# Kernel tuning notes

Hardware: AMD Instinct MI355X
Metric: run time of the kernel (lower is better)

The kernel has to match this reference:

```python
import jax, jax.numpy as jnp
import numpy as np

D_MODEL = 1024
NHEADS = 16
D_K = D_MODEL // NHEADS


def setup_inputs() -> dict:
    key = jax.random.key(0)
    ks = jax.random.split(key, 12)
    B, S = 2, 2048
    scale = 1.0 / np.sqrt(D_MODEL)
    inp = {
        "query": jax.random.normal(ks[0], (B, S, D_MODEL), dtype=jnp.float32),
        "key": jax.random.normal(ks[1], (B, S, D_MODEL), dtype=jnp.float32),
        "value": jax.random.normal(ks[2], (B, S, D_MODEL), dtype=jnp.float32),
        "mask": jax.random.randint(ks[3], (B, 1, S, S), 0, 2, dtype=jnp.int32),
        "Wq": jax.random.normal(ks[4], (D_MODEL, D_MODEL), dtype=jnp.float32) * scale,
        "bq": jnp.zeros((D_MODEL,), dtype=jnp.float32),
        "Wk": jax.random.normal(ks[5], (D_MODEL, D_MODEL), dtype=jnp.float32) * scale,
        "bk": jnp.zeros((D_MODEL,), dtype=jnp.float32),
        "Wv": jax.random.normal(ks[6], (D_MODEL, D_MODEL), dtype=jnp.float32) * scale,
        "bv": jnp.zeros((D_MODEL,), dtype=jnp.float32),
        "Wo": jax.random.normal(ks[7], (D_MODEL, D_MODEL), dtype=jnp.float32) * scale,
        "bo": jnp.zeros((D_MODEL,), dtype=jnp.float32),
    }
    return inp


def _split_heads(x):
    # [B, S, (H*D)] -> [B, H, S, D]
    B, S, _ = x.shape
    return x.reshape(B, S, NHEADS, D_K).transpose(0, 2, 1, 3)


def reference(query, key, value, mask, Wq, bq, Wk, bk, Wv, bv, Wo, bo):
    B, Sq, _ = query.shape
    q = _split_heads(query @ Wq + bq)            # [B, H, Sq, Dk]
    k = _split_heads(key @ Wk + bk)              # [B, H, Sk, Dk]
    v = _split_heads(value @ Wv + bv)            # [B, H, Sk, Dk]
    # scores: [B, H, Sq, Sk], scaled by sqrt(d_k)
    scores = jnp.einsum("bhqd,bhkd->bhqk", q, k) / np.sqrt(D_K).astype(np.float32)
    scores = jnp.where(mask == 0, jnp.float32(-1e12), scores)
    weights = jax.nn.softmax(scores, axis=-1)
    out = jnp.einsum("bhqk,bhkd->bhqd", weights, v)  # [B, H, Sq, Dk]
    out = out.transpose(0, 2, 1, 3).reshape(B, Sq, D_MODEL)
    return out @ Wo + bo  # dropout is identity in eval / p=0
```

## Files before the change

kernel.cpp:

```cpp
#include <hip/hip_runtime.h>
#include <math.h>

#define D_MODEL 1024
#define NHEADS  16
#define DK      64
#define BATCH   2
#define SEQ     2048
#define M_TOTAL (BATCH * SEQ)
#define NT      (SEQ / 64)
#define QSCALE 0.18033688011112042f

typedef __attribute__((ext_vector_type(8))) short bf16x8;
typedef __attribute__((ext_vector_type(4))) float f32x4;

__device__ __forceinline__ unsigned short f2bf(float f) {
    union { float f; unsigned int i; } v; v.f = f;
    return (unsigned short)((v.i + 0x7FFFu + ((v.i >> 16) & 1u)) >> 16);
}

__device__ __forceinline__ void async_copy16(const void* g, void* l) {
    __builtin_amdgcn_global_load_lds(
        (const __attribute__((address_space(1))) unsigned int*)g,
        (__attribute__((address_space(3))) unsigned int*)l, 16, 0, 0);
}

struct PrepArgs {
    const float* xs[3]; unsigned short* xd[3];
    const float* wsrc[4]; unsigned short* wdst[4];
    const int* mask; unsigned long long* wm;
};

__global__ __launch_bounds__(256)
void prep_all(const PrepArgs a)
{
    __shared__ unsigned short tbuf[32][33];
    const int id  = blockIdx.x;
    const int tid = threadIdx.x;

    if (id < 12288) {
        const int z = id >> 12;
        const int x = id & 4095;
        const float* __restrict__ s = a.xs[z];
        unsigned short* __restrict__ d = a.xd[z];
        const size_t i = ((size_t)x * 256 + tid) * 4;
        const float4 v = *reinterpret_cast<const float4*>(&s[i]);
        ushort4 o;
        o.x = f2bf(v.x); o.y = f2bf(v.y); o.z = f2bf(v.z); o.w = f2bf(v.w);
        *reinterpret_cast<ushort4*>(&d[i]) = o;
    } else if (id < 16384) {
        const int r  = id - 12288;
        const int z  = r >> 10;
        const int rem = r & 1023;
        const int bx = rem & 31;
        const int by = rem >> 5;
        const float* __restrict__ W = a.wsrc[z];
        unsigned short* __restrict__ WT = a.wdst[z];
        const int tx = tid & 31;
        const int ty = tid >> 5;
        const int nb = bx << 5;
        const int kb = by << 5;
#pragma unroll
        for (int i = 0; i < 4; ++i)
            tbuf[ty + (i << 3)][tx] =
                f2bf(W[(size_t)(kb + ty + (i << 3)) * D_MODEL + nb + tx]);
        __syncthreads();
#pragma unroll
        for (int i = 0; i < 4; ++i)
            WT[(size_t)(nb + ty + (i << 3)) * D_MODEL + kb + tx] =
                tbuf[tx][ty + (i << 3)];
    } else {
        const int bxm = id - 16384;
        const int lane = tid & 63;
        const int l15  = lane & 15;
        const int kg   = lane >> 4;
        const int wv   = (bxm << 2) + (tid >> 6);
        const int t    = wv & 31;
        const int qw   = (wv >> 5) & 127;
        const int bb   = wv >> 12;

        const int* mb = a.mask + (size_t)bb * SEQ * SEQ
                      + (size_t)((qw << 4) + l15) * SEQ + (t << 6) + (kg << 2);
        unsigned long long* wout = a.wm + ((((size_t)bb * 128 + qw) * 32 + t) << 4);

        int4 ln[4];
#pragma unroll
        for (int n = 0; n < 4; ++n)
            ln[n] = *reinterpret_cast<const int4*>(mb + (n << 4));
#pragma unroll
        for (int r = 0; r < 4; ++r)
#pragma unroll
            for (int n = 0; n < 4; ++n) {
                const int mvv = (&ln[n].x)[r];
                const unsigned long long bal = __ballot(mvv != 0);
                if (lane == 0) wout[(r << 2) | n] = bal;
            }
    }
}

template <typename OutT> struct GArgs {
    const unsigned short* X[3];
    const unsigned short* W[3];
    const float*          Bi[3];
    OutT*                 O[3];
    float                 scl[3];
};

__device__ __forceinline__ void st_out(float* p, float v) { *p = v; }
__device__ __forceinline__ void st_out(unsigned short* p, float v) { *p = f2bf(v); }

template <typename OutT>
__global__ __launch_bounds__(256)
void gemm_bf16(const GArgs<OutT> args, const int head_split, const int m_z_tiles)
{
    __shared__ __align__(16) unsigned short As[128][32];
    __shared__ __align__(16) unsigned short Bs[128][32];

    const int opz = m_z_tiles ? 0 : blockIdx.z;
    const unsigned short* __restrict__ X  = args.X[opz];
    const unsigned short* __restrict__ WT = args.W[opz];
    const float* __restrict__ bias        = args.Bi[opz];
    OutT* __restrict__ out                = args.O[opz];
    const float scl                       = args.scl[opz];

    const int tid = threadIdx.x;
    const int wid = tid >> 6;
    const int wy  = wid >> 1;
    const int wx  = wid & 1;
    const int l15 = tid & 15;
    const int kg  = (tid >> 4) & 3;

    const int nwgy = (int)gridDim.y;
    const int id = ((int)blockIdx.y << 3) | (int)blockIdx.x;
    const int sw = (id & 7) * nwgy + (id >> 3);
    const int n0 = (sw & 7) << 7;
    const int m0 = ((sw >> 3) + (int)blockIdx.z * m_z_tiles) << 7;

    const int lane = tid & 63;
    const int gr   = lane >> 2;
    const int gc   = (lane & 3) << 3;
    const int c0   = wid << 1;

    f32x4 acc[4][4];
#pragma unroll
    for (int i = 0; i < 4; ++i)
#pragma unroll
        for (int j = 0; j < 4; ++j)
            acc[i][j] = (f32x4){0.f, 0.f, 0.f, 0.f};

#pragma unroll 1
    for (int t = 0; t < D_MODEL / 32; ++t) {
        const int k0 = t << 5;

        __syncthreads();
#pragma unroll
        for (int cc = 0; cc < 2; ++cc) {
            const int c = c0 + cc;
            async_copy16(&X[(size_t)(m0 + (c << 4) + gr) * D_MODEL + k0 + gc],
                         &As[c << 4][0]);
            async_copy16(&WT[(size_t)(n0 + (c << 4) + gr) * D_MODEL + k0 + gc],
                         &Bs[c << 4][0]);
        }
        __syncthreads();

        bf16x8 a[4], b[4];
#pragma unroll
        for (int i = 0; i < 4; ++i)
            a[i] = *reinterpret_cast<const bf16x8*>(
                &As[(wy << 6) + (i << 4) + l15][kg << 3]);
#pragma unroll
        for (int j = 0; j < 4; ++j)
            b[j] = *reinterpret_cast<const bf16x8*>(
                &Bs[(wx << 6) + (j << 4) + l15][kg << 3]);
#pragma unroll
        for (int i = 0; i < 4; ++i)
#pragma unroll
            for (int j = 0; j < 4; ++j)
                acc[i][j] = __builtin_amdgcn_mfma_f32_16x16x32_bf16(
                    a[i], b[j], acc[i][j], 0, 0, 0);
    }

    float bv[4];
#pragma unroll
    for (int j = 0; j < 4; ++j)
        bv[j] = bias[n0 + (wx << 6) + (j << 4) + l15];

#pragma unroll
    for (int i = 0; i < 4; ++i) {
#pragma unroll
        for (int r = 0; r < 4; ++r) {
            const int m = m0 + (wy << 6) + (i << 4) + (kg << 2) + r;
#pragma unroll
            for (int j = 0; j < 4; ++j) {
                const int n = n0 + (wx << 6) + (j << 4) + l15;
                const float val = (acc[i][j][r] + bv[j]) * scl;
                if (head_split) {
                    const int bbx = m >> 11;
                    const int ss  = m & (SEQ - 1);
                    const int hhx = n >> 6;
                    const int dd  = n & (DK - 1);
                    st_out(&out[((size_t)(bbx * NHEADS + hhx) * SEQ + ss) * DK + dd], val);
                } else {
                    st_out(&out[(size_t)m * D_MODEL + n], val);
                }
            }
        }
    }
}

__global__ __launch_bounds__(256)
void flash_mfma(const unsigned short* __restrict__ Qb,
                const unsigned short* __restrict__ Kb,
                const unsigned short* __restrict__ Vb,
                const unsigned long long* __restrict__ wmask,
                unsigned short* __restrict__ ctx)
{
    __shared__ __align__(16) unsigned short Kbf[2][64][72];
    __shared__ __align__(16) unsigned short V3 [2][64][72];

    const int tid  = threadIdx.x;
    const int w    = tid >> 6;
    const int lane = tid & 63;
    const int l15  = lane & 15;
    const int kg   = lane >> 4;

    const int flat = ((int)blockIdx.z * NHEADS + (int)blockIdx.y) * (SEQ / 128)
                   + (int)blockIdx.x;
    const int swz  = ((flat & 7) << 6) | (flat >> 3);
    const int q0 = (swz & 15) << 7;
    const int hh = (swz >> 4) & 15;
    const int bb = swz >> 8;

    const unsigned short* Qh = Qb + (size_t)(bb * NHEADS + hh) * SEQ * DK;
    const unsigned short* Kh = Kb + (size_t)(bb * NHEADS + hh) * SEQ * DK;
    const unsigned short* Vh = Vb + (size_t)(bb * NHEADS + hh) * SEQ * DK;

    bf16x8 aq[2][2];
#pragma unroll
    for (int qi = 0; qi < 2; ++qi) {
        const unsigned short* qrow =
            Qh + (size_t)(q0 + w * 32 + qi * 16 + l15) * DK + (kg << 3);
        aq[qi][0] = *reinterpret_cast<const bf16x8*>(qrow);
        aq[qi][1] = *reinterpret_cast<const bf16x8*>(qrow + 32);
    }

    const int krow = tid >> 2;
    const int kcb  = (tid & 3) << 4;
    const int vkb  = (tid & 15) << 2;
    const int vdb  = (tid >> 4) << 2;
    const int voff = (((vkb >> 2) & 3) << 4) + ((vkb >> 4) << 2);

    const int wbase0 = __builtin_amdgcn_readfirstlane(
        (bb * 128 + (q0 >> 4) + (w << 1)) << 9);
    const int wbase1 = wbase0 + 512;

    f32x4 lsum[2];
    f32x4 O4[2][4];
#pragma unroll
    for (int qi = 0; qi < 2; ++qi) {
        lsum[qi] = (f32x4){0.f, 0.f, 0.f, 0.f};
#pragma unroll
        for (int db = 0; db < 4; ++db) O4[qi][db] = (f32x4){0.f, 0.f, 0.f, 0.f};
    }

    uint4 kv0 = *reinterpret_cast<const uint4*>(Kh + (size_t)krow * DK + kcb);
    uint4 kv1 = *reinterpret_cast<const uint4*>(Kh + (size_t)krow * DK + kcb + 8);
    uint2 vr[4];
#pragma unroll
    for (int i = 0; i < 4; ++i)
        vr[i] = *reinterpret_cast<const uint2*>(Vh + (size_t)(vkb + i) * DK + vdb);

#pragma unroll 1
    for (int t = 0; t < NT; ++t) {
        const int c = t & 1;

        *reinterpret_cast<uint4*>(&Kbf[c][krow][kcb])     = kv0;
        *reinterpret_cast<uint4*>(&Kbf[c][krow][kcb + 8]) = kv1;
        {
            uint2 o;
            o.x = (vr[0].x & 0xFFFFu) | (vr[1].x << 16);
            o.y = (vr[2].x & 0xFFFFu) | (vr[3].x << 16);
            *reinterpret_cast<uint2*>(&V3[c][vdb + 0][voff]) = o;
            o.x = (vr[0].x >> 16) | (vr[1].x & 0xFFFF0000u);
            o.y = (vr[2].x >> 16) | (vr[3].x & 0xFFFF0000u);
            *reinterpret_cast<uint2*>(&V3[c][vdb + 1][voff]) = o;
            o.x = (vr[0].y & 0xFFFFu) | (vr[1].y << 16);
            o.y = (vr[2].y & 0xFFFFu) | (vr[3].y << 16);
            *reinterpret_cast<uint2*>(&V3[c][vdb + 2][voff]) = o;
            o.x = (vr[0].y >> 16) | (vr[1].y & 0xFFFF0000u);
            o.y = (vr[2].y >> 16) | (vr[3].y & 0xFFFF0000u);
            *reinterpret_cast<uint2*>(&V3[c][vdb + 3][voff]) = o;
        }
        __syncthreads();

        if (t + 1 < NT) {
            const int kn = (t + 1) << 6;
            kv0 = *reinterpret_cast<const uint4*>(Kh + (size_t)(kn + krow) * DK + kcb);
            kv1 = *reinterpret_cast<const uint4*>(Kh + (size_t)(kn + krow) * DK + kcb + 8);
#pragma unroll
            for (int i = 0; i < 4; ++i)
                vr[i] = *reinterpret_cast<const uint2*>(
                    Vh + (size_t)(kn + vkb + i) * DK + vdb);
        }

        f32x4 S[2][4];
#pragma unroll
        for (int n = 0; n < 4; ++n) {
            const bf16x8 b0 = *reinterpret_cast<const bf16x8*>(
                &Kbf[c][16 * n + l15][kg << 3]);
            const bf16x8 b1 = *reinterpret_cast<const bf16x8*>(
                &Kbf[c][16 * n + l15][(kg << 3) + 32]);
#pragma unroll
            for (int qi = 0; qi < 2; ++qi) {
                f32x4 acc = (f32x4){0.f, 0.f, 0.f, 0.f};
                acc = __builtin_amdgcn_mfma_f32_16x16x32_bf16(b0, aq[qi][0], acc, 0, 0, 0);
                acc = __builtin_amdgcn_mfma_f32_16x16x32_bf16(b1, aq[qi][1], acc, 0, 0, 0);
                S[qi][n] = acc;
            }
        }

        bf16x8 paf[2][2];
#pragma unroll
        for (int qi = 0; qi < 2; ++qi) {
            const unsigned long long* wmt =
                wmask + (qi ? wbase1 : wbase0) + (t << 4);
            unsigned long long wmv[16];
#pragma unroll
            for (int rn = 0; rn < 16; ++rn) wmv[rn] = wmt[rn];

            unsigned pw01[4], pw23[4];
#pragma unroll
            for (int n = 0; n < 4; ++n) {
                float xv[4];
#pragma unroll
                for (int r = 0; r < 4; ++r) {
                    float e;
                    __asm__("v_exp_f32 %0, %1" : "=v"(e) : "v"(S[qi][n][r]));
                    __asm__("v_cndmask_b32 %0, 0, %1, %2"
                            : "=v"(e) : "v"(e), "s"(wmv[(r << 2) | n]));
                    xv[r] = e;
                }
                lsum[qi][0] += xv[0];
                lsum[qi][1] += xv[1];
                lsum[qi][2] += xv[2];
                lsum[qi][3] += xv[3];
                __asm__("v_cvt_pk_bf16_f32 %0, %1, %2"
                        : "=v"(pw01[n]) : "v"(xv[0]), "v"(xv[1]));
                __asm__("v_cvt_pk_bf16_f32 %0, %1, %2"
                        : "=v"(pw23[n]) : "v"(xv[2]), "v"(xv[3]));
            }
            union { unsigned u[4]; bf16x8 v; } pa0, pa1;
            pa0.u[0] = pw01[0]; pa0.u[1] = pw23[0]; pa0.u[2] = pw01[1]; pa0.u[3] = pw23[1];
            pa1.u[0] = pw01[2]; pa1.u[1] = pw23[2]; pa1.u[2] = pw01[3]; pa1.u[3] = pw23[3];
            paf[qi][0] = pa0.v;
            paf[qi][1] = pa1.v;
        }

#pragma unroll
        for (int db = 0; db < 4; ++db) {
            const unsigned short* vbase = &V3[c][(db << 4) + l15][kg << 4];
            const bf16x8 v0 = *reinterpret_cast<const bf16x8*>(vbase);
            const bf16x8 v1 = *reinterpret_cast<const bf16x8*>(vbase + 8);
#pragma unroll
            for (int qi = 0; qi < 2; ++qi) {
                O4[qi][db] = __builtin_amdgcn_mfma_f32_16x16x32_bf16(
                    paf[qi][0], v0, O4[qi][db], 0, 0, 0);
                O4[qi][db] = __builtin_amdgcn_mfma_f32_16x16x32_bf16(
                    paf[qi][1], v1, O4[qi][db], 0, 0, 0);
            }
        }
    }

#pragma unroll
    for (int qi = 0; qi < 2; ++qi) {
        float ls = (lsum[qi][0] + lsum[qi][1]) + (lsum[qi][2] + lsum[qi][3]);
        ls += __shfl_xor(ls, 16);
        ls += __shfl_xor(ls, 32);
#pragma unroll
        for (int r = 0; r < 4; ++r) {
            const float rs = __shfl(ls, (kg << 2) + r);
            const float inv = 1.f / rs;
            const size_t base =
                (size_t)(bb * SEQ + q0 + w * 32 + qi * 16 + (kg << 2) + r) * D_MODEL
                + hh * DK + l15;
#pragma unroll
            for (int db = 0; db < 4; ++db)
                ctx[base + 16 * db] = f2bf(O4[qi][db][r] * inv);
        }
    }
}

extern "C" void kernel_launch(void* const* d_in, const int* in_sizes, int n_in,
                              void* d_out, int out_size, void* d_ws, size_t ws_size,
                              hipStream_t stream)
{
    const float* query = (const float*)d_in[0];
    const float* key   = (const float*)d_in[1];
    const float* value = (const float*)d_in[2];
    const int*   mask  = (const int*)d_in[3];
    const float* Wq = (const float*)d_in[4];
    const float* bq = (const float*)d_in[5];
    const float* Wk = (const float*)d_in[6];
    const float* bk = (const float*)d_in[7];
    const float* Wv = (const float*)d_in[8];
    const float* bv = (const float*)d_in[9];
    const float* Wo = (const float*)d_in[10];
    const float* bo = (const float*)d_in[11];

    unsigned short* ws = (unsigned short*)d_ws;
    const size_t TE = (size_t)M_TOTAL * D_MODEL;
    const size_t WE = (size_t)D_MODEL * D_MODEL;
    unsigned short* Xq  = ws;
    unsigned short* Xk  = Xq + TE;
    unsigned short* Xv  = Xk + TE;
    unsigned short* WTq = Xv + TE;
    unsigned short* WTk = WTq + WE;
    unsigned short* WTv = WTk + WE;
    unsigned short* WTo = WTv + WE;
    unsigned short* Qb  = WTo + WE;
    unsigned short* Kb  = Qb + TE;
    unsigned short* Vb  = Kb + TE;
    unsigned short* Ctx = Vb + TE;
    unsigned long long* WM = (unsigned long long*)(Ctx + TE);

    PrepArgs pa;
    pa.xs[0] = query; pa.xs[1] = key; pa.xs[2] = value;
    pa.xd[0] = Xq;    pa.xd[1] = Xk;  pa.xd[2] = Xv;
    pa.wsrc[0] = Wq;  pa.wsrc[1] = Wk;  pa.wsrc[2] = Wv;  pa.wsrc[3] = Wo;
    pa.wdst[0] = WTq; pa.wdst[1] = WTk; pa.wdst[2] = WTv; pa.wdst[3] = WTo;
    pa.mask = mask; pa.wm = WM;
    prep_all<<<dim3(18432, 1, 1), 256, 0, stream>>>(pa);

    GArgs<unsigned short> qkv;
    qkv.X[0] = Xq;  qkv.X[1] = Xk;  qkv.X[2] = Xv;
    qkv.W[0] = WTq; qkv.W[1] = WTk; qkv.W[2] = WTv;
    qkv.Bi[0] = bq; qkv.Bi[1] = bk; qkv.Bi[2] = bv;
    qkv.O[0] = Qb;  qkv.O[1] = Kb;  qkv.O[2] = Vb;
    qkv.scl[0] = QSCALE; qkv.scl[1] = 1.f; qkv.scl[2] = 1.f;
    gemm_bf16<unsigned short><<<dim3(8, 32, 3), 256, 0, stream>>>(qkv, 1, 0);

    flash_mfma<<<dim3(SEQ / 128, NHEADS, BATCH), 256, 0, stream>>>(
        Qb, Kb, Vb, WM, Ctx);

    GArgs<float> op;
    op.X[0] = Ctx;  op.X[1] = Ctx;  op.X[2] = Ctx;
    op.W[0] = WTo;  op.W[1] = WTo;  op.W[2] = WTo;
    op.Bi[0] = bo;  op.Bi[1] = bo;  op.Bi[2] = bo;
    op.O[0] = (float*)d_out; op.O[1] = (float*)d_out; op.O[2] = (float*)d_out;
    op.scl[0] = 1.f; op.scl[1] = 1.f; op.scl[2] = 1.f;
    gemm_bf16<float><<<dim3(8, 16, 2), 256, 0, stream>>>(op, 0, 16);
}
```

Measured before the change: 266.0 us.

## Stage 128-key tiles in flash attention and use 64-row tiles for output GEMM

The attention kernel now loads and stages 128 keys per loop iteration, not 64. It halves the number of barriers and loop iterations and prefetches larger K/V blocks, at the cost of more LDS and registers. The GEMM is templated on the number of M sub-tiles, and the output projection uses 64x128 tiles with a single z-slice. This gives twice as many workgroups for better CU occupancy, but each one reuses less data.

New measurement: 258.7 us. 2.8% less time.

```diff
diff --git a/kernel.cpp b/kernel.cpp
--- a/kernel.cpp
+++ b/kernel.cpp
@@ -7,7 +7,7 @@
 #define BATCH   2
 #define SEQ     2048
 #define M_TOTAL (BATCH * SEQ)
-#define NT      (SEQ / 64)
+#define NT128   (SEQ / 128)
 #define QSCALE 0.18033688011112042f
 
 typedef __attribute__((ext_vector_type(8))) short bf16x8;
@@ -108,14 +108,14 @@
 __device__ __forceinline__ void st_out(float* p, float v) { *p = v; }
 __device__ __forceinline__ void st_out(unsigned short* p, float v) { *p = f2bf(v); }
 
-template <typename OutT>
+template <typename OutT, int MI>
 __global__ __launch_bounds__(256)
-void gemm_bf16(const GArgs<OutT> args, const int head_split, const int m_z_tiles)
+void gemm_bf16(const GArgs<OutT> args, const int head_split)
 {
-    __shared__ __align__(16) unsigned short As[128][32];
+    __shared__ __align__(16) unsigned short As[MI * 32][32];
     __shared__ __align__(16) unsigned short Bs[128][32];
 
-    const int opz = m_z_tiles ? 0 : blockIdx.z;
+    const int opz = blockIdx.z;
     const unsigned short* __restrict__ X  = args.X[opz];
     const unsigned short* __restrict__ WT = args.W[opz];
     const float* __restrict__ bias        = args.Bi[opz];
@@ -133,16 +133,15 @@
     const int id = ((int)blockIdx.y << 3) | (int)blockIdx.x;
     const int sw = (id & 7) * nwgy + (id >> 3);
     const int n0 = (sw & 7) << 7;
-    const int m0 = ((sw >> 3) + (int)blockIdx.z * m_z_tiles) << 7;
+    const int m0 = (sw >> 3) * (MI * 32);
 
     const int lane = tid & 63;
     const int gr   = lane >> 2;
     const int gc   = (lane & 3) << 3;
-    const int c0   = wid << 1;
-
-    f32x4 acc[4][4];
-#pragma unroll
-    for (int i = 0; i < 4; ++i)
+
+    f32x4 acc[MI][4];
+#pragma unroll
+    for (int i = 0; i < MI; ++i)
 #pragma unroll
         for (int j = 0; j < 4; ++j)
             acc[i][j] = (f32x4){0.f, 0.f, 0.f, 0.f};
@@ -154,25 +153,29 @@
         __syncthreads();
 #pragma unroll
         for (int cc = 0; cc < 2; ++cc) {
-            const int c = c0 + cc;
-            async_copy16(&X[(size_t)(m0 + (c << 4) + gr) * D_MODEL + k0 + gc],
-                         &As[c << 4][0]);
+            const int c = (wid << 1) + cc;
             async_copy16(&WT[(size_t)(n0 + (c << 4) + gr) * D_MODEL + k0 + gc],
                          &Bs[c << 4][0]);
-        }
+            if (MI == 4)
+                async_copy16(&X[(size_t)(m0 + (c << 4) + gr) * D_MODEL + k0 + gc],
+                             &As[c << 4][0]);
+        }
+        if (MI == 2)
+            async_copy16(&X[(size_t)(m0 + (wid << 4) + gr) * D_MODEL + k0 + gc],
+                         &As[wid << 4][0]);
         __syncthreads();
 
-        bf16x8 a[4], b[4];
-#pragma unroll
-        for (int i = 0; i < 4; ++i)
+        bf16x8 a[MI], b[4];
+#pragma unroll
+        for (int i = 0; i < MI; ++i)
             a[i] = *reinterpret_cast<const bf16x8*>(
-                &As[(wy << 6) + (i << 4) + l15][kg << 3]);
+                &As[(wy * MI + i) * 16 + l15][kg << 3]);
 #pragma unroll
         for (int j = 0; j < 4; ++j)
             b[j] = *reinterpret_cast<const bf16x8*>(
                 &Bs[(wx << 6) + (j << 4) + l15][kg << 3]);
 #pragma unroll
-        for (int i = 0; i < 4; ++i)
+        for (int i = 0; i < MI; ++i)
 #pragma unroll
             for (int j = 0; j < 4; ++j)
                 acc[i][j] = __builtin_amdgcn_mfma_f32_16x16x32_bf16(
@@ -185,10 +188,10 @@
         bv[j] = bias[n0 + (wx << 6) + (j << 4) + l15];
 
 #pragma unroll
-    for (int i = 0; i < 4; ++i) {
+    for (int i = 0; i < MI; ++i) {
 #pragma unroll
         for (int r = 0; r < 4; ++r) {
-            const int m = m0 + (wy << 6) + (i << 4) + (kg << 2) + r;
+            const int m = m0 + (wy * MI + i) * 16 + (kg << 2) + r;
 #pragma unroll
             for (int j = 0; j < 4; ++j) {
                 const int n = n0 + (wx << 6) + (j << 4) + l15;
@@ -214,8 +217,8 @@
                 const unsigned long long* __restrict__ wmask,
                 unsigned short* __restrict__ ctx)
 {
-    __shared__ __align__(16) unsigned short Kbf[2][64][72];
-    __shared__ __align__(16) unsigned short V3 [2][64][72];
+    __shared__ __align__(16) unsigned short Kbf[2][128][72];
+    __shared__ __align__(16) unsigned short V3 [2][64][136];
 
     const int tid  = threadIdx.x;
     const int w    = tid >> 6;
@@ -247,7 +250,8 @@
     const int kcb  = (tid & 3) << 4;
     const int vkb  = (tid & 15) << 2;
     const int vdb  = (tid >> 4) << 2;
-    const int voff = (((vkb >> 2) & 3) << 4) + ((vkb >> 4) << 2);
+    const int q16  = tid & 15;
+    const int voff = ((q16 & 3) << 5) | ((q16 >> 2) << 2);
 
     const int wbase0 = __builtin_amdgcn_readfirstlane(
         (bb * 128 + (q0 >> 4) + (w << 1)) << 9);
@@ -262,110 +266,128 @@
         for (int db = 0; db < 4; ++db) O4[qi][db] = (f32x4){0.f, 0.f, 0.f, 0.f};
     }
 
-    uint4 kv0 = *reinterpret_cast<const uint4*>(Kh + (size_t)krow * DK + kcb);
-    uint4 kv1 = *reinterpret_cast<const uint4*>(Kh + (size_t)krow * DK + kcb + 8);
-    uint2 vr[4];
-#pragma unroll
-    for (int i = 0; i < 4; ++i)
-        vr[i] = *reinterpret_cast<const uint2*>(Vh + (size_t)(vkb + i) * DK + vdb);
+    uint4 kv0a = *reinterpret_cast<const uint4*>(Kh + (size_t)krow * DK + kcb);
+    uint4 kv1a = *reinterpret_cast<const uint4*>(Kh + (size_t)krow * DK + kcb + 8);
+    uint4 kv0b = *reinterpret_cast<const uint4*>(Kh + (size_t)(krow + 64) * DK + kcb);
+    uint4 kv1b = *reinterpret_cast<const uint4*>(Kh + (size_t)(krow + 64) * DK + kcb + 8);
+    uint2 vra[4], vrb[4];
+#pragma unroll
+    for (int i = 0; i < 4; ++i) {
+        vra[i] = *reinterpret_cast<const uint2*>(Vh + (size_t)(vkb + i) * DK + vdb);
+        vrb[i] = *reinterpret_cast<const uint2*>(Vh + (size_t)(64 + vkb + i) * DK + vdb);
+    }
 
 #pragma unroll 1
-    for (int t = 0; t < NT; ++t) {
+    for (int t = 0; t < NT128; ++t) {
         const int c = t & 1;
 
-        *reinterpret_cast<uint4*>(&Kbf[c][krow][kcb])     = kv0;
-        *reinterpret_cast<uint4*>(&Kbf[c][krow][kcb + 8]) = kv1;
-        {
+        *reinterpret_cast<uint4*>(&Kbf[c][krow][kcb])          = kv0a;
+        *reinterpret_cast<uint4*>(&Kbf[c][krow][kcb + 8])      = kv1a;
+        *reinterpret_cast<uint4*>(&Kbf[c][krow + 64][kcb])     = kv0b;
+        *reinterpret_cast<uint4*>(&Kbf[c][krow + 64][kcb + 8]) = kv1b;
+#pragma unroll
+        for (int hf = 0; hf < 2; ++hf) {
+            const uint2* vr = hf ? vrb : vra;
+            const int vo = voff + (hf << 4);
             uint2 o;
             o.x = (vr[0].x & 0xFFFFu) | (vr[1].x << 16);
             o.y = (vr[2].x & 0xFFFFu) | (vr[3].x << 16);
-            *reinterpret_cast<uint2*>(&V3[c][vdb + 0][voff]) = o;
+            *reinterpret_cast<uint2*>(&V3[c][vdb + 0][vo]) = o;
             o.x = (vr[0].x >> 16) | (vr[1].x & 0xFFFF0000u);
             o.y = (vr[2].x >> 16) | (vr[3].x & 0xFFFF0000u);
-            *reinterpret_cast<uint2*>(&V3[c][vdb + 1][voff]) = o;
+            *reinterpret_cast<uint2*>(&V3[c][vdb + 1][vo]) = o;
             o.x = (vr[0].y & 0xFFFFu) | (vr[1].y << 16);
             o.y = (vr[2].y & 0xFFFFu) | (vr[3].y << 16);
-            *reinterpret_cast<uint2*>(&V3[c][vdb + 2][voff]) = o;
+            *reinterpret_cast<uint2*>(&V3[c][vdb + 2][vo]) = o;
             o.x = (vr[0].y >> 16) | (vr[1].y & 0xFFFF0000u);
             o.y = (vr[2].y >> 16) | (vr[3].y & 0xFFFF0000u);
-            *reinterpret_cast<uint2*>(&V3[c][vdb + 3][voff]) = o;
+            *reinterpret_cast<uint2*>(&V3[c][vdb + 3][vo]) = o;
         }
         __syncthreads();
 
-        if (t + 1 < NT) {
-            const int kn = (t + 1) << 6;
-            kv0 = *reinterpret_cast<const uint4*>(Kh + (size_t)(kn + krow) * DK + kcb);
-            kv1 = *reinterpret_cast<const uint4*>(Kh + (size_t)(kn + krow) * DK + kcb + 8);
-#pragma unroll
-            for (int i = 0; i < 4; ++i)
-                vr[i] = *reinterpret_cast<const uint2*>(
+        if (t + 1 < NT128) {
+            const int kn = (t + 1) << 7;
+            kv0a = *reinterpret_cast<const uint4*>(Kh + (size_t)(kn + krow) * DK + kcb);
+            kv1a = *reinterpret_cast<const uint4*>(Kh + (size_t)(kn + krow) * DK + kcb + 8);
+            kv0b = *reinterpret_cast<const uint4*>(Kh + (size_t)(kn + krow + 64) * DK + kcb);
+            kv1b = *reinterpret_cast<const uint4*>(Kh + (size_t)(kn + krow + 64) * DK + kcb + 8);
+#pragma unroll
+            for (int i = 0; i < 4; ++i) {
+                vra[i] = *reinterpret_cast<const uint2*>(
                     Vh + (size_t)(kn + vkb + i) * DK + vdb);
-        }
-
-        f32x4 S[2][4];
-#pragma unroll
-        for (int n = 0; n < 4; ++n) {
-            const bf16x8 b0 = *reinterpret_cast<const bf16x8*>(
-                &Kbf[c][16 * n + l15][kg << 3]);
-            const bf16x8 b1 = *reinterpret_cast<const bf16x8*>(
-                &Kbf[c][16 * n + l15][(kg << 3) + 32]);
+                vrb[i] = *reinterpret_cast<const uint2*>(
+                    Vh + (size_t)(kn + 64 + vkb + i) * DK + vdb);
+            }
+        }
+
+#pragma unroll
+        for (int h = 0; h < 2; ++h) {
+            f32x4 S[2][4];
+#pragma unroll
+            for (int n = 0; n < 4; ++n) {
+                const bf16x8 b0 = *reinterpret_cast<const bf16x8*>(
+                    &Kbf[c][(h << 6) + 16 * n + l15][kg << 3]);
+                const bf16x8 b1 = *reinterpret_cast<const bf16x8*>(
+                    &Kbf[c][(h << 6) + 16 * n + l15][(kg << 3) + 32]);
+#pragma unroll
+                for (int qi = 0; qi < 2; ++qi) {
+                    f32x4 acc = (f32x4){0.f, 0.f, 0.f, 0.f};
+                    acc = __builtin_amdgcn_mfma_f32_16x16x32_bf16(b0, aq[qi][0], acc, 0, 0, 0);
+                    acc = __builtin_amdgcn_mfma_f32_16x16x32_bf16(b1, aq[qi][1], acc, 0, 0, 0);
+                    S[qi][n] = acc;
+                }
+            }
+
+            bf16x8 paf[2][2];
 #pragma unroll
             for (int qi = 0; qi < 2; ++qi) {
-                f32x4 acc = (f32x4){0.f, 0.f, 0.f, 0.f};
-                acc = __builtin_amdgcn_mfma_f32_16x16x32_bf16(b0, aq[qi][0], acc, 0, 0, 0);
-                acc = __builtin_amdgcn_mfma_f32_16x16x32_bf16(b1, aq[qi][1], acc, 0, 0, 0);
-                S[qi][n] = acc;
-            }
-        }
-
-        bf16x8 paf[2][2];
-#pragma unroll
-        for (int qi = 0; qi < 2; ++qi) {
-            const unsigned long long* wmt =
-                wmask + (qi ? wbase1 : wbase0) + (t << 4);
-            unsigned long long wmv[16];
-#pragma unroll
-            for (int rn = 0; rn < 16; ++rn) wmv[rn] = wmt[rn];
-
-            unsigned pw01[4], pw23[4];
-#pragma unroll
-            for (int n = 0; n < 4; ++n) {
-                float xv[4];
-#pragma unroll
-                for (int r = 0; r < 4; ++r) {
-                    float e;
-                    __asm__("v_exp_f32 %0, %1" : "=v"(e) : "v"(S[qi][n][r]));
-                    __asm__("v_cndmask_b32 %0, 0, %1, %2"
-                            : "=v"(e) : "v"(e), "s"(wmv[(r << 2) | n]));
-                    xv[r] = e;
+                const unsigned long long* wmt =
+                    wmask + (qi ? wbase1 : wbase0) + (((t << 1) | h) << 4);
+                unsigned long long wmv[16];
+#pragma unroll
+                for (int rn = 0; rn < 16; ++rn) wmv[rn] = wmt[rn];
+
+                unsigned pw01[4], pw23[4];
+#pragma unroll
+                for (int n = 0; n < 4; ++n) {
+                    float xv[4];
+#pragma unroll
+                    for (int r = 0; r < 4; ++r) {
+                        float e;
+                        __asm__("v_exp_f32 %0, %1" : "=v"(e) : "v"(S[qi][n][r]));
+                        __asm__("v_cndmask_b32 %0, 0, %1, %2"
+                                : "=v"(e) : "v"(e), "s"(wmv[(r << 2) | n]));
+                        xv[r] = e;
+                    }
+                    lsum[qi][0] += xv[0];
+                    lsum[qi][1] += xv[1];
+                    lsum[qi][2] += xv[2];
+                    lsum[qi][3] += xv[3];
+                    __asm__("v_cvt_pk_bf16_f32 %0, %1, %2"
+                            : "=v"(pw01[n]) : "v"(xv[0]), "v"(xv[1]));
+                    __asm__("v_cvt_pk_bf16_f32 %0, %1, %2"
+                            : "=v"(pw23[n]) : "v"(xv[2]), "v"(xv[3]));
                 }
-                lsum[qi][0] += xv[0];
-                lsum[qi][1] += xv[1];
-                lsum[qi][2] += xv[2];
-                lsum[qi][3] += xv[3];
-                __asm__("v_cvt_pk_bf16_f32 %0, %1, %2"
-                        : "=v"(pw01[n]) : "v"(xv[0]), "v"(xv[1]));
-                __asm__("v_cvt_pk_bf16_f32 %0, %1, %2"
-                        : "=v"(pw23[n]) : "v"(xv[2]), "v"(xv[3]));
-            }
-            union { unsigned u[4]; bf16x8 v; } pa0, pa1;
-            pa0.u[0] = pw01[0]; pa0.u[1] = pw23[0]; pa0.u[2] = pw01[1]; pa0.u[3] = pw23[1];
-            pa1.u[0] = pw01[2]; pa1.u[1] = pw23[2]; pa1.u[2] = pw01[3]; pa1.u[3] = pw23[3];
-            paf[qi][0] = pa0.v;
-            paf[qi][1] = pa1.v;
-        }
-
-#pragma unroll
-        for (int db = 0; db < 4; ++db) {
-            const unsigned short* vbase = &V3[c][(db << 4) + l15][kg << 4];
-            const bf16x8 v0 = *reinterpret_cast<const bf16x8*>(vbase);
-            const bf16x8 v1 = *reinterpret_cast<const bf16x8*>(vbase + 8);
-#pragma unroll
-            for (int qi = 0; qi < 2; ++qi) {
-                O4[qi][db] = __builtin_amdgcn_mfma_f32_16x16x32_bf16(
-                    paf[qi][0], v0, O4[qi][db], 0, 0, 0);
-                O4[qi][db] = __builtin_amdgcn_mfma_f32_16x16x32_bf16(
-                    paf[qi][1], v1, O4[qi][db], 0, 0, 0);
+                union { unsigned u[4]; bf16x8 v; } pa0, pa1;
+                pa0.u[0] = pw01[0]; pa0.u[1] = pw23[0]; pa0.u[2] = pw01[1]; pa0.u[3] = pw23[1];
+                pa1.u[0] = pw01[2]; pa1.u[1] = pw23[2]; pa1.u[2] = pw01[3]; pa1.u[3] = pw23[3];
+                paf[qi][0] = pa0.v;
+                paf[qi][1] = pa1.v;
+            }
+
+#pragma unroll
+            for (int db = 0; db < 4; ++db) {
+                const unsigned short* vbase =
+                    &V3[c][(db << 4) + l15][(kg << 5) | (h << 4)];
+                const bf16x8 v0 = *reinterpret_cast<const bf16x8*>(vbase);
+                const bf16x8 v1 = *reinterpret_cast<const bf16x8*>(vbase + 8);
+#pragma unroll
+                for (int qi = 0; qi < 2; ++qi) {
+                    O4[qi][db] = __builtin_amdgcn_mfma_f32_16x16x32_bf16(
+                        paf[qi][0], v0, O4[qi][db], 0, 0, 0);
+                    O4[qi][db] = __builtin_amdgcn_mfma_f32_16x16x32_bf16(
+                        paf[qi][1], v1, O4[qi][db], 0, 0, 0);
+                }
             }
         }
     }
@@ -436,7 +458,7 @@
     qkv.Bi[0] = bq; qkv.Bi[1] = bk; qkv.Bi[2] = bv;
     qkv.O[0] = Qb;  qkv.O[1] = Kb;  qkv.O[2] = Vb;
     qkv.scl[0] = QSCALE; qkv.scl[1] = 1.f; qkv.scl[2] = 1.f;
-    gemm_bf16<unsigned short><<<dim3(8, 32, 3), 256, 0, stream>>>(qkv, 1, 0);
+    gemm_bf16<unsigned short, 4><<<dim3(8, 32, 3), 256, 0, stream>>>(qkv, 1);
 
     flash_mfma<<<dim3(SEQ / 128, NHEADS, BATCH), 256, 0, stream>>>(
         Qb, Kb, Vb, WM, Ctx);
@@ -447,5 +469,5 @@
     op.Bi[0] = bo;  op.Bi[1] = bo;  op.Bi[2] = bo;
     op.O[0] = (float*)d_out; op.O[1] = (float*)d_out; op.O[2] = (float*)d_out;
     op.scl[0] = 1.f; op.scl[1] = 1.f; op.scl[2] = 1.f;
-    gemm_bf16<float><<<dim3(8, 16, 2), 256, 0, stream>>>(op, 0, 16);
-}
+    gemm_bf16<float, 2><<<dim3(8, 64, 1), 256, 0, stream>>>(op, 0);
+}
```
